# Kernel optimization log

Measured on AMD Instinct MI355X. Metric: run time of the kernel, lower is better.

## Reference

```python
import jax, jax.numpy as jnp
import numpy as np

N_NODES = 100000
N_EDGES = 1600000
IN_FEATS = 128
OUT_FEATS = 128


def setup_inputs() -> dict:
    key = jax.random.key(0)
    k1, k2, k3, k4, k5 = jax.random.split(key, 5)
    feat = jax.random.normal(k1, (N_NODES, IN_FEATS), dtype=jnp.float32)
    # He (kaiming) uniform-ish init scale for the weights
    bound = np.sqrt(6.0 / IN_FEATS).astype(np.float32)
    weight_u = jax.random.uniform(k2, (IN_FEATS, OUT_FEATS), jnp.float32, -bound, bound)
    weight_v = jax.random.uniform(k3, (IN_FEATS, OUT_FEATS), jnp.float32, -bound, bound)
    bias = jnp.zeros((OUT_FEATS,), dtype=jnp.float32)
    src = jax.random.randint(k4, (N_EDGES,), 0, N_NODES, dtype=jnp.int32)
    dst = jax.random.randint(k5, (N_EDGES,), 0, N_NODES, dtype=jnp.int32)
    return {"feat": feat, "weight_u": weight_u, "weight_v": weight_v,
            "bias": bias, "src": src, "dst": dst}


def reference(feat, weight_u, weight_v, bias, src, dst):
    n = feat.shape[0]
    # in_feats (128) is not > out_feats (128) -> aggregate first, then matmul
    # m_i = sum_{j in N(i)} h_j  (copy_u + sum over edges)
    agg = jax.ops.segment_sum(feat[src], dst, num_segments=n)  # [N, in_feats]
    rst_u = jnp.matmul(agg, weight_u)                          # [N, out_feats]
    rst_v = jnp.matmul(feat, weight_v)                         # [N, out_feats]
    # in-degree normalization, clamped at 1
    deg = jax.ops.segment_sum(jnp.ones_like(dst, dtype=feat.dtype), dst,
                              num_segments=n)
    norm = 1.0 / jnp.maximum(deg, 1.0)                         # [N]
    out = jax.nn.relu(rst_v + norm[:, None] * rst_u + bias)
    return out
```

## Files before the change

kernel.cpp:

```cpp
#include <hip/hip_runtime.h>
#include <hip/hip_bf16.h>
#include <stdint.h>

#define NN 100000
#define NE 1600000
#define NF 128
#define NTILE ((NN + 63) / 64)
#define B_BKT 1563
#define NB2 128
#define EPB (NE / NB2)
#define NCNT (B_BKT * NB2)
#define SC2A ((NCNT + 255) / 256)

typedef __attribute__((ext_vector_type(8))) __bf16 bf16x8;
typedef __attribute__((ext_vector_type(4))) float floatx4;
typedef __attribute__((ext_vector_type(4))) unsigned short ushortx4;
typedef __attribute__((ext_vector_type(8))) unsigned short ushortx8;

static __device__ __forceinline__ unsigned short f2bf(float x) {
    union { float f; unsigned u; } v; v.f = x;
    unsigned r = v.u + 0x7fffu + ((v.u >> 16) & 1u);
    return (unsigned short)(r >> 16);
}
static __device__ __forceinline__ float bflo(unsigned w) {
    union { unsigned u; float f; } v; v.u = w << 16; return v.f;
}
static __device__ __forceinline__ float bfhi(unsigned w) {
    union { unsigned u; float f; } v; v.u = w & 0xffff0000u; return v.f;
}

__global__ void k_convert(const float* __restrict__ s, unsigned short* __restrict__ d, int n4) {
    int i = blockIdx.x * blockDim.x + threadIdx.x;
    if (i < n4) {
        floatx4 f = __builtin_nontemporal_load((const floatx4*)s + i);
        ushortx4 o;
        o.x = f2bf(f.x); o.y = f2bf(f.y); o.z = f2bf(f.z); o.w = f2bf(f.w);
        ((ushortx4*)d)[i] = o;
    }
}

__global__ void k_prep(const float* __restrict__ wv, const float* __restrict__ wu,
                       unsigned short* __restrict__ w2t) {
    int id = blockIdx.x * 256 + threadIdx.x;
    if (id >= 128 * 32) return;
    int n = id >> 5, kg = id & 31;
    const float* srcm = (kg < 16) ? wv : wu;
    int k0 = (kg & 15) * 8;
    ushortx8 o;
#pragma unroll
    for (int j = 0; j < 8; ++j)
        o[j] = f2bf(srcm[(k0 + j) * 128 + n]);
    int dchunk = n * 32 + (kg ^ (n & 7));
    *(ushortx8*)(w2t + dchunk * 8) = o;
}

__global__ void k_count(const int* __restrict__ dst, int* __restrict__ counts) {
    __shared__ int h[B_BKT];
    int tid = threadIdx.x;
    for (int i = tid; i < B_BKT; i += 256) h[i] = 0;
    __syncthreads();
    int base = blockIdx.x * EPB, end = base + EPB;
    for (int i = base + tid; i < end; i += 256) {
        int d = __builtin_nontemporal_load(&dst[i]);
        atomicAdd(&h[d >> 6], 1);
    }
    __syncthreads();
    for (int i = tid; i < B_BKT; i += 256)
        counts[i * NB2 + blockIdx.x] = h[i];
}

__global__ void k_scan2_a(int* __restrict__ counts, int* __restrict__ bsums) {
    __shared__ int sh[256];
    int i = blockIdx.x * 256 + threadIdx.x;
    int v = (i < NCNT) ? counts[i] : 0;
    sh[threadIdx.x] = v;
    __syncthreads();
    for (int off = 1; off < 256; off <<= 1) {
        int u = (threadIdx.x >= off) ? sh[threadIdx.x - off] : 0;
        __syncthreads();
        sh[threadIdx.x] += u;
        __syncthreads();
    }
    if (i < NCNT) counts[i] = sh[threadIdx.x] - v;
    if (threadIdx.x == 255) bsums[blockIdx.x] = sh[255];
}
__global__ void k_scan2_b(int* __restrict__ bsums) {
    __shared__ int sh[1024];
    int t = threadIdx.x;
    int v = (t < SC2A) ? bsums[t] : 0;
    sh[t] = v;
    __syncthreads();
    for (int off = 1; off < 1024; off <<= 1) {
        int u = (t >= off) ? sh[t - off] : 0;
        __syncthreads();
        sh[t] += u;
        __syncthreads();
    }
    if (t < SC2A) bsums[t] = sh[t] - v;
}
__global__ void k_scan2_c(int* __restrict__ counts, const int* __restrict__ bsums) {
    int i = blockIdx.x * 256 + threadIdx.x;
    if (i < NCNT) counts[i] += bsums[blockIdx.x];
}

__global__ void k_binscatter(const int* __restrict__ src, const int* __restrict__ dst,
                             const int* __restrict__ counts, unsigned* __restrict__ streams) {
    __shared__ int cur[B_BKT];
    int tid = threadIdx.x;
    for (int i = tid; i < B_BKT; i += 256)
        cur[i] = counts[i * NB2 + blockIdx.x];
    __syncthreads();
    int base = blockIdx.x * EPB, end = base + EPB;
    for (int i = base + tid; i < end; i += 256) {
        int d = __builtin_nontemporal_load(&dst[i]);
        int s = __builtin_nontemporal_load(&src[i]);
        int b = d >> 6;
        unsigned packed = ((unsigned)(d & 63) << 17) | (unsigned)s;
        int pos = atomicAdd(&cur[b], 1);
        streams[pos] = packed;
    }
}

__global__ void k_csr(const unsigned* __restrict__ streams,
                      const int* __restrict__ counts,
                      int* __restrict__ offs, int* __restrict__ csr) {
    __shared__ int hist[64];
    __shared__ int nodeoff[65];
    int tid = threadIdx.x;
    int bkt = blockIdx.x;
    int s = counts[bkt * NB2];
    int e = (bkt == B_BKT - 1) ? NE : counts[(bkt + 1) * NB2];
    if (tid < 64) hist[tid] = 0;
    __syncthreads();
    for (int i = s + tid; i < e; i += 256)
        atomicAdd(&hist[streams[i] >> 17], 1);
    __syncthreads();
    if (tid == 0) {
        int run = 0;
#pragma unroll
        for (int n = 0; n < 64; ++n) { nodeoff[n] = run; run += hist[n]; }
        nodeoff[64] = run;
    }
    __syncthreads();
    if (tid < 64) {
        int node = bkt * 64 + tid;
        if (node < NN) offs[node] = s + nodeoff[tid];
        hist[tid] = nodeoff[tid];
    }
    if (bkt == B_BKT - 1 && tid == 0) offs[NN] = NE;
    __syncthreads();
    for (int i = s + tid; i < e; i += 256) {
        unsigned v = streams[i];
        int p = atomicAdd(&hist[v >> 17], 1);
        csr[s + p] = (int)(v & 0x1FFFFu);
    }
}

__global__ void k_aggregate(const unsigned short* __restrict__ featb,
                            const int* __restrict__ offs,
                            const int* __restrict__ csr,
                            unsigned short* __restrict__ aggb) {
    int lane = threadIdx.x & 63;
    int node = blockIdx.x * 4 + (threadIdx.x >> 6);
    if (node >= NN) return;
    int s0 = offs[node], s1 = offs[node + 1];
    float a0 = 0.f, a1 = 0.f;
    for (int base = s0; base < s1; base += 64) {
        int e = (base + lane < s1) ? csr[base + lane] : 0;
        int m = s1 - base; if (m > 64) m = 64;
        int j = 0;
        for (; j + 8 <= m; j += 8) {
            unsigned w0 = *(const unsigned*)(featb + (size_t)__shfl(e, j + 0, 64) * NF + lane * 2);
            unsigned w1 = *(const unsigned*)(featb + (size_t)__shfl(e, j + 1, 64) * NF + lane * 2);
            unsigned w2 = *(const unsigned*)(featb + (size_t)__shfl(e, j + 2, 64) * NF + lane * 2);
            unsigned w3 = *(const unsigned*)(featb + (size_t)__shfl(e, j + 3, 64) * NF + lane * 2);
            unsigned w4 = *(const unsigned*)(featb + (size_t)__shfl(e, j + 4, 64) * NF + lane * 2);
            unsigned w5 = *(const unsigned*)(featb + (size_t)__shfl(e, j + 5, 64) * NF + lane * 2);
            unsigned w6 = *(const unsigned*)(featb + (size_t)__shfl(e, j + 6, 64) * NF + lane * 2);
            unsigned w7 = *(const unsigned*)(featb + (size_t)__shfl(e, j + 7, 64) * NF + lane * 2);
            a0 += bflo(w0) + bflo(w1) + bflo(w2) + bflo(w3)
                + bflo(w4) + bflo(w5) + bflo(w6) + bflo(w7);
            a1 += bfhi(w0) + bfhi(w1) + bfhi(w2) + bfhi(w3)
                + bfhi(w4) + bfhi(w5) + bfhi(w6) + bfhi(w7);
        }
        for (; j < m; ++j) {
            int nn = __shfl(e, j, 64);
            unsigned w = *(const unsigned*)(featb + (size_t)nn * NF + lane * 2);
            a0 += bflo(w); a1 += bfhi(w);
        }
    }
    int dg = s1 - s0; if (dg < 1) dg = 1;
    float scale = 1.0f / (float)dg;
    unsigned outw = ((unsigned)f2bf(a1 * scale) << 16) | (unsigned)f2bf(a0 * scale);
    *(unsigned*)(aggb + (size_t)node * NF + lane * 2) = outw;
}

__global__ __launch_bounds__(256, 2) void k_gemm(
    const unsigned short* __restrict__ featb,
    const unsigned short* __restrict__ aggb,
    const unsigned short* __restrict__ w2t,
    const float* __restrict__ bias,
    float* __restrict__ out) {
    __shared__ unsigned short lds[128 * 256];
    for (int i = threadIdx.x; i < 4096; i += 256) {
        ushortx8 w = *(const ushortx8*)(w2t + i * 8);
        *(ushortx8*)(&lds[i * 8]) = w;
    }
    __syncthreads();

    int lane = threadIdx.x & 63;
    int wave = threadIdx.x >> 6;
    int quad = lane >> 4, l15 = lane & 15;

    float bsv[8];
#pragma unroll
    for (int ct = 0; ct < 8; ++ct) bsv[ct] = bias[ct * 16 + l15];

    for (int t = blockIdx.x; t < NTILE; t += gridDim.x) {
        int rb = t * 64 + wave * 16;
        int arow = rb + l15; if (arow > NN - 1) arow = NN - 1;
        const unsigned short* fr = featb + (size_t)arow * NF;
        const unsigned short* ar = aggb + (size_t)arow * NF;
        bf16x8 a[8];
#pragma unroll
        for (int ks = 0; ks < 4; ++ks) {
            a[ks]     = *(const bf16x8*)(fr + ks * 32 + quad * 8);
            a[4 + ks] = *(const bf16x8*)(ar + ks * 32 + quad * 8);
        }
        floatx4 acc[8];
#pragma unroll
        for (int ct = 0; ct < 8; ++ct) acc[ct] = (floatx4){0.f, 0.f, 0.f, 0.f};
#pragma unroll
        for (int ct = 0; ct < 8; ++ct) {
            int n = ct * 16 + l15;
            int rowoff = n << 8;
            int sw = n & 7;
#pragma unroll
            for (int ks = 0; ks < 8; ++ks) {
                int kg = ks * 4 + quad;
                bf16x8 b = *(const bf16x8*)(&lds[rowoff + ((kg ^ sw) << 3)]);
                acc[ct] = __builtin_amdgcn_mfma_f32_16x16x32_bf16(a[ks], b, acc[ct], 0, 0, 0);
            }
        }
#pragma unroll
        for (int ct = 0; ct < 8; ++ct) {
            int col = ct * 16 + l15;
#pragma unroll
            for (int r = 0; r < 4; ++r) {
                int row = rb + quad * 4 + r;
                if (row < NN) {
                    float v = acc[ct][r] + bsv[ct];
                    out[(size_t)row * NF + col] = v > 0.f ? v : 0.f;
                }
            }
        }
    }
}

extern "C" void kernel_launch(void* const* d_in, const int* in_sizes, int n_in,
                              void* d_out, int out_size, void* d_ws, size_t ws_size,
                              hipStream_t stream) {
    const float* feat = (const float*)d_in[0];
    const float* wu   = (const float*)d_in[1];
    const float* wv   = (const float*)d_in[2];
    const float* bias = (const float*)d_in[3];
    const int* src    = (const int*)d_in[4];
    const int* dst    = (const int*)d_in[5];
    float* out        = (float*)d_out;

    char* ws = (char*)d_ws;
    int* counts           = (int*)(ws + 0);
    int* bsums            = (int*)(ws + 800256);
    int* offs             = (int*)(ws + 804352);
    int* csr              = (int*)(ws + 1204480);
    unsigned short* featb = (unsigned short*)(ws + 7604480);
    unsigned short* aggb  = (unsigned short*)(ws + 33204480);
    unsigned short* w2t   = (unsigned short*)(ws + 58804480);
    unsigned* streams     = (unsigned*)aggb;

    k_convert<<<(NN * NF / 4 + 255) / 256, 256, 0, stream>>>(feat, featb, NN * NF / 4);
    k_prep<<<16, 256, 0, stream>>>(wv, wu, w2t);

    k_count<<<NB2, 256, 0, stream>>>(dst, counts);
    k_scan2_a<<<SC2A, 256, 0, stream>>>(counts, bsums);
    k_scan2_b<<<1, 1024, 0, stream>>>(bsums);
    k_scan2_c<<<SC2A, 256, 0, stream>>>(counts, bsums);
    k_binscatter<<<NB2, 256, 0, stream>>>(src, dst, counts, streams);
    k_csr<<<B_BKT, 256, 0, stream>>>(streams, counts, offs, csr);
    k_aggregate<<<(NN + 3) / 4, 256, 0, stream>>>(featb, offs, csr, aggb);
    k_gemm<<<768, 256, 0, stream>>>(featb, aggb, w2t, bias, out);
}
```

Baseline: 314.6 us.

## Merge setup kernels, fold scan fixup into consumers, restructure GEMM tiles

Merges the feature conversion, weight prep and dst counting into one launch, and drops the scan fixup kernel by adding block sums inside binscatter and csr. Binscatter now runs 512-thread blocks. The GEMM uses exactly two tiles per block and loads both A tiles up front so their memory latency overlaps. Fewer launches and less global traffic are traded for higher register pressure in the GEMM.

```diff
diff --git a/kernel.cpp b/kernel.cpp
--- a/kernel.cpp
+++ b/kernel.cpp
@@ -6,11 +6,15 @@
 #define NE 1600000
 #define NF 128
 #define NTILE ((NN + 63) / 64)
+#define GEMM_G 782
 #define B_BKT 1563
 #define NB2 128
 #define EPB (NE / NB2)
 #define NCNT (B_BKT * NB2)
 #define SC2A ((NCNT + 255) / 256)
+#define CONV4 (NN * NF / 4)
+#define CONV_BLK ((CONV4 + 255) / 256)
+#define SETUP_GRID (NB2 + 16 + CONV_BLK)
 
 typedef __attribute__((ext_vector_type(8))) __bf16 bf16x8;
 typedef __attribute__((ext_vector_type(4))) float floatx4;
@@ -29,44 +33,46 @@
     union { unsigned u; float f; } v; v.u = w & 0xffff0000u; return v.f;
 }
 
-__global__ void k_convert(const float* __restrict__ s, unsigned short* __restrict__ d, int n4) {
-    int i = blockIdx.x * blockDim.x + threadIdx.x;
-    if (i < n4) {
-        floatx4 f = __builtin_nontemporal_load((const floatx4*)s + i);
-        ushortx4 o;
-        o.x = f2bf(f.x); o.y = f2bf(f.y); o.z = f2bf(f.z); o.w = f2bf(f.w);
-        ((ushortx4*)d)[i] = o;
-    }
-}
-
-__global__ void k_prep(const float* __restrict__ wv, const float* __restrict__ wu,
-                       unsigned short* __restrict__ w2t) {
-    int id = blockIdx.x * 256 + threadIdx.x;
-    if (id >= 128 * 32) return;
-    int n = id >> 5, kg = id & 31;
-    const float* srcm = (kg < 16) ? wv : wu;
-    int k0 = (kg & 15) * 8;
-    ushortx8 o;
-#pragma unroll
-    for (int j = 0; j < 8; ++j)
-        o[j] = f2bf(srcm[(k0 + j) * 128 + n]);
-    int dchunk = n * 32 + (kg ^ (n & 7));
-    *(ushortx8*)(w2t + dchunk * 8) = o;
-}
-
-__global__ void k_count(const int* __restrict__ dst, int* __restrict__ counts) {
+__global__ void k_setup(const float* __restrict__ feat, unsigned short* __restrict__ featb,
+                        const float* __restrict__ wv, const float* __restrict__ wu,
+                        unsigned short* __restrict__ w2t,
+                        const int* __restrict__ dst, int* __restrict__ counts) {
     __shared__ int h[B_BKT];
+    int b = blockIdx.x;
     int tid = threadIdx.x;
-    for (int i = tid; i < B_BKT; i += 256) h[i] = 0;
-    __syncthreads();
-    int base = blockIdx.x * EPB, end = base + EPB;
-    for (int i = base + tid; i < end; i += 256) {
-        int d = __builtin_nontemporal_load(&dst[i]);
-        atomicAdd(&h[d >> 6], 1);
-    }
-    __syncthreads();
-    for (int i = tid; i < B_BKT; i += 256)
-        counts[i * NB2 + blockIdx.x] = h[i];
+    if (b < NB2) {
+        for (int i = tid; i < B_BKT; i += 256) h[i] = 0;
+        __syncthreads();
+        int base = b * EPB, end = base + EPB;
+        for (int i = base + tid; i < end; i += 256) {
+            int d = __builtin_nontemporal_load(&dst[i]);
+            atomicAdd(&h[d >> 6], 1);
+        }
+        __syncthreads();
+        for (int i = tid; i < B_BKT; i += 256)
+            counts[i * NB2 + b] = h[i];
+    } else if (b < NB2 + 16) {
+        int id = (b - NB2) * 256 + tid;
+        if (id < 128 * 32) {
+            int n = id >> 5, kg = id & 31;
+            const float* srcm = (kg < 16) ? wv : wu;
+            int k0 = (kg & 15) * 8;
+            ushortx8 o;
+#pragma unroll
+            for (int j = 0; j < 8; ++j)
+                o[j] = f2bf(srcm[(k0 + j) * 128 + n]);
+            int dchunk = n * 32 + (kg ^ (n & 7));
+            *(ushortx8*)(w2t + dchunk * 8) = o;
+        }
+    } else {
+        int i = (b - NB2 - 16) * 256 + tid;
+        if (i < CONV4) {
+            floatx4 f = __builtin_nontemporal_load((const floatx4*)feat + i);
+            ushortx4 o;
+            o.x = f2bf(f.x); o.y = f2bf(f.y); o.z = f2bf(f.z); o.w = f2bf(f.w);
+            __builtin_nontemporal_store(o, (ushortx4*)featb + i);
+        }
+    }
 }
 
 __global__ void k_scan2_a(int* __restrict__ counts, int* __restrict__ bsums) {
@@ -98,20 +104,19 @@
     }
     if (t < SC2A) bsums[t] = sh[t] - v;
 }
-__global__ void k_scan2_c(int* __restrict__ counts, const int* __restrict__ bsums) {
-    int i = blockIdx.x * 256 + threadIdx.x;
-    if (i < NCNT) counts[i] += bsums[blockIdx.x];
-}
 
 __global__ void k_binscatter(const int* __restrict__ src, const int* __restrict__ dst,
-                             const int* __restrict__ counts, unsigned* __restrict__ streams) {
+                             const int* __restrict__ counts, const int* __restrict__ bsums,
+                             unsigned* __restrict__ streams) {
     __shared__ int cur[B_BKT];
     int tid = threadIdx.x;
-    for (int i = tid; i < B_BKT; i += 256)
-        cur[i] = counts[i * NB2 + blockIdx.x];
+    for (int i = tid; i < B_BKT; i += 512) {
+        int idx = i * NB2 + blockIdx.x;
+        cur[i] = counts[idx] + bsums[idx >> 8];
+    }
     __syncthreads();
     int base = blockIdx.x * EPB, end = base + EPB;
-    for (int i = base + tid; i < end; i += 256) {
+    for (int i = base + tid; i < end; i += 512) {
         int d = __builtin_nontemporal_load(&dst[i]);
         int s = __builtin_nontemporal_load(&src[i]);
         int b = d >> 6;
@@ -122,14 +127,15 @@
 }
 
 __global__ void k_csr(const unsigned* __restrict__ streams,
-                      const int* __restrict__ counts,
+                      const int* __restrict__ counts, const int* __restrict__ bsums,
                       int* __restrict__ offs, int* __restrict__ csr) {
     __shared__ int hist[64];
     __shared__ int nodeoff[65];
     int tid = threadIdx.x;
     int bkt = blockIdx.x;
-    int s = counts[bkt * NB2];
-    int e = (bkt == B_BKT - 1) ? NE : counts[(bkt + 1) * NB2];
+    int idx = bkt * NB2;
+    int s = counts[idx] + bsums[idx >> 8];
+    int e = (bkt == B_BKT - 1) ? NE : (counts[idx + NB2] + bsums[(idx + NB2) >> 8]);
     if (tid < 64) hist[tid] = 0;
     __syncthreads();
     for (int i = s + tid; i < e; i += 256)
@@ -195,6 +201,38 @@
     *(unsigned*)(aggb + (size_t)node * NF + lane * 2) = outw;
 }
 
+static __device__ __forceinline__ void gemm_tile(
+    const unsigned short* lds, const bf16x8* a, const float* bsv,
+    int rb, int quad, int l15, float* __restrict__ out) {
+    floatx4 acc[8];
+#pragma unroll
+    for (int ct = 0; ct < 8; ++ct) acc[ct] = (floatx4){0.f, 0.f, 0.f, 0.f};
+#pragma unroll
+    for (int ct = 0; ct < 8; ++ct) {
+        int n = ct * 16 + l15;
+        int rowoff = n << 8;
+        int sw = n & 7;
+#pragma unroll
+        for (int ks = 0; ks < 8; ++ks) {
+            int kg = ks * 4 + quad;
+            bf16x8 b = *(const bf16x8*)(&lds[rowoff + ((kg ^ sw) << 3)]);
+            acc[ct] = __builtin_amdgcn_mfma_f32_16x16x32_bf16(a[ks], b, acc[ct], 0, 0, 0);
+        }
+    }
+#pragma unroll
+    for (int r = 0; r < 4; ++r) {
+        int row = rb + quad * 4 + r;
+        if (row < NN) {
+#pragma unroll
+            for (int ct = 0; ct < 8; ++ct) {
+                int col = ct * 16 + l15;
+                float v = acc[ct][r] + bsv[ct];
+                out[(size_t)row * NF + col] = v > 0.f ? v : 0.f;
+            }
+        }
+    }
+}
+
 __global__ __launch_bounds__(256, 2) void k_gemm(
     const unsigned short* __restrict__ featb,
     const unsigned short* __restrict__ aggb,
@@ -216,45 +254,34 @@
 #pragma unroll
     for (int ct = 0; ct < 8; ++ct) bsv[ct] = bias[ct * 16 + l15];
 
-    for (int t = blockIdx.x; t < NTILE; t += gridDim.x) {
-        int rb = t * 64 + wave * 16;
-        int arow = rb + l15; if (arow > NN - 1) arow = NN - 1;
-        const unsigned short* fr = featb + (size_t)arow * NF;
-        const unsigned short* ar = aggb + (size_t)arow * NF;
-        bf16x8 a[8];
-#pragma unroll
-        for (int ks = 0; ks < 4; ++ks) {
-            a[ks]     = *(const bf16x8*)(fr + ks * 32 + quad * 8);
-            a[4 + ks] = *(const bf16x8*)(ar + ks * 32 + quad * 8);
-        }
-        floatx4 acc[8];
-#pragma unroll
-        for (int ct = 0; ct < 8; ++ct) acc[ct] = (floatx4){0.f, 0.f, 0.f, 0.f};
-#pragma unroll
-        for (int ct = 0; ct < 8; ++ct) {
-            int n = ct * 16 + l15;
-            int rowoff = n << 8;
-            int sw = n & 7;
-#pragma unroll
-            for (int ks = 0; ks < 8; ++ks) {
-                int kg = ks * 4 + quad;
-                bf16x8 b = *(const bf16x8*)(&lds[rowoff + ((kg ^ sw) << 3)]);
-                acc[ct] = __builtin_amdgcn_mfma_f32_16x16x32_bf16(a[ks], b, acc[ct], 0, 0, 0);
-            }
-        }
-#pragma unroll
-        for (int ct = 0; ct < 8; ++ct) {
-            int col = ct * 16 + l15;
-#pragma unroll
-            for (int r = 0; r < 4; ++r) {
-                int row = rb + quad * 4 + r;
-                if (row < NN) {
-                    float v = acc[ct][r] + bsv[ct];
-                    out[(size_t)row * NF + col] = v > 0.f ? v : 0.f;
-                }
-            }
-        }
-    }
+    int t0 = blockIdx.x;
+    int t1 = t0 + GEMM_G;
+    int t1v = (t1 < NTILE) ? t1 : t0;
+
+    int rb0 = t0 * 64 + wave * 16;
+    int rb1 = t1v * 64 + wave * 16;
+    int ar0 = rb0 + l15; if (ar0 > NN - 1) ar0 = NN - 1;
+    int ar1 = rb1 + l15; if (ar1 > NN - 1) ar1 = NN - 1;
+    const unsigned short* fr0 = featb + (size_t)ar0 * NF;
+    const unsigned short* ag0 = aggb + (size_t)ar0 * NF;
+    const unsigned short* fr1 = featb + (size_t)ar1 * NF;
+    const unsigned short* ag1 = aggb + (size_t)ar1 * NF;
+
+    bf16x8 a0[8], a1[8];
+#pragma unroll
+    for (int ks = 0; ks < 4; ++ks) {
+        a0[ks]     = *(const bf16x8*)(fr0 + ks * 32 + quad * 8);
+        a0[4 + ks] = *(const bf16x8*)(ag0 + ks * 32 + quad * 8);
+    }
+#pragma unroll
+    for (int ks = 0; ks < 4; ++ks) {
+        a1[ks]     = *(const bf16x8*)(fr1 + ks * 32 + quad * 8);
+        a1[4 + ks] = *(const bf16x8*)(ag1 + ks * 32 + quad * 8);
+    }
+
+    gemm_tile(lds, a0, bsv, rb0, quad, l15, out);
+    if (t1 < NTILE)
+        gemm_tile(lds, a1, bsv, rb1, quad, l15, out);
 }
 
 extern "C" void kernel_launch(void* const* d_in, const int* in_sizes, int n_in,
@@ -278,15 +305,11 @@
     unsigned short* w2t   = (unsigned short*)(ws + 58804480);
     unsigned* streams     = (unsigned*)aggb;
 
-    k_convert<<<(NN * NF / 4 + 255) / 256, 256, 0, stream>>>(feat, featb, NN * NF / 4);
-    k_prep<<<16, 256, 0, stream>>>(wv, wu, w2t);
-
-    k_count<<<NB2, 256, 0, stream>>>(dst, counts);
+    k_setup<<<SETUP_GRID, 256, 0, stream>>>(feat, featb, wv, wu, w2t, dst, counts);
     k_scan2_a<<<SC2A, 256, 0, stream>>>(counts, bsums);
     k_scan2_b<<<1, 1024, 0, stream>>>(bsums);
-    k_scan2_c<<<SC2A, 256, 0, stream>>>(counts, bsums);
-    k_binscatter<<<NB2, 256, 0, stream>>>(src, dst, counts, streams);
-    k_csr<<<B_BKT, 256, 0, stream>>>(streams, counts, offs, csr);
+    k_binscatter<<<NB2, 512, 0, stream>>>(src, dst, counts, bsums, streams);
+    k_csr<<<B_BKT, 256, 0, stream>>>(streams, counts, bsums, offs, csr);
     k_aggregate<<<(NN + 3) / 4, 256, 0, stream>>>(featb, offs, csr, aggb);
-    k_gemm<<<768, 256, 0, stream>>>(featb, aggb, w2t, bias, out);
-}
+    k_gemm<<<GEMM_G, 256, 0, stream>>>(featb, aggb, w2t, bias, out);
+}
```

New measurement: 295.1 us. 1.07x faster.
